# Performance work log

Measured on AMD Instinct MI355X. Metric: run time of the kernel, lower is better.

The kernel has to match this reference:

```python
import jax, jax.numpy as jnp
import numpy as np

TOP_K = 2

def setup_inputs() -> dict:
    key = jax.random.key(0)
    k0, k1, k2, k3 = jax.random.split(key, 4)
    B, S, H, I, E = 2, 2048, 1024, 1408, 8
    hidden_states = jax.random.normal(k0, (B, S, H), dtype=jnp.float32)
    router_weight = jax.random.normal(k1, (E, H), dtype=jnp.float32) * 0.02
    gate_up_proj = jax.random.normal(k2, (E, 2 * I, H), dtype=jnp.float32) * 0.02
    down_proj = jax.random.normal(k3, (E, H, I), dtype=jnp.float32) * 0.02
    return {
        "hidden_states": hidden_states,
        "router_weight": router_weight,
        "gate_up_proj": gate_up_proj,
        "down_proj": down_proj,
    }

def reference(hidden_states, router_weight, gate_up_proj, down_proj):
    B, S, H = hidden_states.shape
    E = router_weight.shape[0]
    x = hidden_states.reshape(-1, H)                       # [T, H]
    T = x.shape[0]
    # Router: logits -> float32 softmax -> top-k (matches torch: topk on probs)
    logits = x @ router_weight.T                           # [T, E]
    probs = jax.nn.softmax(logits.astype(jnp.float32), axis=-1)
    topw, topi = jax.lax.top_k(probs, TOP_K)               # [T, K]
    topw = topw.astype(x.dtype)
    # Per-token combine weights over experts (zero for non-selected experts).
    combine = jnp.zeros((T, E), dtype=x.dtype)
    combine = combine.at[jnp.arange(T)[:, None], topi].set(topw)  # [T, E]
    # Dense grouped expert compute (same math as gather-GEMM-scatter loop:
    # tokens not routed to expert e get combine weight 0).
    gu = jnp.einsum('th,eoh->teo', x, gate_up_proj)        # [T, E, 2I]
    g, u = jnp.split(gu, 2, axis=-1)                       # [T, E, I] each
    h = jax.nn.silu(g) * u                                 # [T, E, I]
    y = jnp.einsum('tei,ehi->teh', h, down_proj)           # [T, E, H]
    out = jnp.einsum('teh,te->th', y, combine)             # [T, H]
    return out.reshape(B, S, H)
```

## Files before the change

kernel.cpp:

```cpp
#include <hip/hip_runtime.h>
#include <math.h>

#define NTOK 4096
#define HDIM 1024
#define NEXP 8
#define IDIM 1408
#define TWO_I 2816
#define BM 128
#define BK 32
#define NRB 72
#define ROWCAP (NRB * BM)

typedef _Float16 f16x8 __attribute__((ext_vector_type(8)));
typedef float f32x4 __attribute__((ext_vector_type(4)));

typedef __attribute__((address_space(1))) const unsigned int gu32;
typedef __attribute__((address_space(3))) unsigned int lu32;
__device__ __forceinline__ void async16(const void* g, void* l) {
  __builtin_amdgcn_global_load_lds((gu32*)g, (lu32*)l, 16, 0, 0);
}

extern "C" __global__ void moe_init(int* counts, int* cursor, int* tok) {
  int i = blockIdx.x * 256 + threadIdx.x;
  if (i < NEXP) { counts[i] = 0; cursor[i] = 0; }
  if (i < ROWCAP) tok[i] = -1;
}

extern "C" __global__ void moe_cvt(const float* __restrict__ src, _Float16* __restrict__ dst, int n8) {
  int i = blockIdx.x * 256 + threadIdx.x;
  if (i >= n8) return;
  const float4* s = (const float4*)src + (size_t)i * 2;
  float4 a = s[0], b = s[1];
  union { _Float16 h[8]; uint4 u; } p;
  p.h[0] = (_Float16)a.x; p.h[1] = (_Float16)a.y; p.h[2] = (_Float16)a.z; p.h[3] = (_Float16)a.w;
  p.h[4] = (_Float16)b.x; p.h[5] = (_Float16)b.y; p.h[6] = (_Float16)b.z; p.h[7] = (_Float16)b.w;
  ((uint4*)dst)[i] = p.u;
}

extern "C" __global__ void moe_router(const float* __restrict__ x,
                                      const float* __restrict__ rw,
                                      int* __restrict__ topi,
                                      float* __restrict__ topw) {
  int w = threadIdx.x >> 6, lane = threadIdx.x & 63;
  int t = blockIdx.x * 4 + w;
  const float4* xp = (const float4*)(x + (size_t)t * HDIM);
  const float4* rp = (const float4*)rw;
  float acc[NEXP];
#pragma unroll
  for (int e = 0; e < NEXP; e++) acc[e] = 0.f;
#pragma unroll
  for (int i = 0; i < HDIM / 256; i++) {
    float4 xv = xp[i * 64 + lane];
#pragma unroll
    for (int e = 0; e < NEXP; e++) {
      float4 rv = rp[e * 256 + i * 64 + lane];
      acc[e] += xv.x * rv.x + xv.y * rv.y + xv.z * rv.z + xv.w * rv.w;
    }
  }
#pragma unroll
  for (int e = 0; e < NEXP; e++) {
#pragma unroll
    for (int off = 32; off > 0; off >>= 1) acc[e] += __shfl_down(acc[e], off);
  }
  if (lane == 0) {
    float m = acc[0];
    for (int e = 1; e < NEXP; e++) m = fmaxf(m, acc[e]);
    float p[NEXP], s = 0.f;
    for (int e = 0; e < NEXP; e++) { p[e] = __expf(acc[e] - m); s += p[e]; }
    float inv = 1.f / s;
    int i0 = 0; float b0 = p[0];
    for (int e = 1; e < NEXP; e++) if (p[e] > b0) { b0 = p[e]; i0 = e; }
    int i1 = -1; float b1 = -1.f;
    for (int e = 0; e < NEXP; e++) if (e != i0 && p[e] > b1) { b1 = p[e]; i1 = e; }
    topi[t * 2] = i0; topi[t * 2 + 1] = i1;
    topw[t * 2] = b0 * inv; topw[t * 2 + 1] = b1 * inv;
  }
}

extern "C" __global__ void moe_count(const int* __restrict__ topi, int* __restrict__ counts) {
  __shared__ int cnt[NEXP];
  if (threadIdx.x < NEXP) cnt[threadIdx.x] = 0;
  __syncthreads();
  int t = blockIdx.x * 256 + threadIdx.x;
  atomicAdd(&cnt[topi[t * 2]], 1);
  atomicAdd(&cnt[topi[t * 2 + 1]], 1);
  __syncthreads();
  if (threadIdx.x < NEXP) atomicAdd(&counts[threadIdx.x], cnt[threadIdx.x]);
}

extern "C" __global__ void moe_offsets(const int* __restrict__ counts, int* __restrict__ aoff) {
  if (threadIdx.x == 0) {
    int o = 0;
    aoff[0] = 0;
    for (int e = 0; e < NEXP; e++) {
      o += ((counts[e] + BM - 1) / BM) * BM;
      aoff[e + 1] = o;
    }
  }
}

extern "C" __global__ void moe_scatter(const int* __restrict__ topi, const float* __restrict__ topw,
                                       const int* __restrict__ aoff, int* __restrict__ cursor,
                                       int* __restrict__ tok, float* __restrict__ wrow,
                                       int* __restrict__ rows) {
  __shared__ int cnt[NEXP];
  __shared__ int base[NEXP];
  int tid = threadIdx.x;
  if (tid < NEXP) cnt[tid] = 0;
  __syncthreads();
  int t = blockIdx.x * 256 + tid;
  int e0 = topi[t * 2], e1 = topi[t * 2 + 1];
  int r0 = atomicAdd(&cnt[e0], 1);
  int r1 = atomicAdd(&cnt[e1], 1);
  __syncthreads();
  if (tid < NEXP) base[tid] = atomicAdd(&cursor[tid], cnt[tid]);
  __syncthreads();
  int row0 = aoff[e0] + base[e0] + r0;
  int row1 = aoff[e1] + base[e1] + r1;
  tok[row0] = t; wrow[row0] = topw[t * 2];     rows[t * 2]     = row0;
  tok[row1] = t; wrow[row1] = topw[t * 2 + 1]; rows[t * 2 + 1] = row1;
}

union SM1 {
  struct { _Float16 a[BM * BK]; _Float16 b[BM * BK]; } st;
  _Float16 ubuf[BM * 66];
};

extern "C" __global__ __launch_bounds__(256) void moe_gemm1(
    const _Float16* __restrict__ xh, const _Float16* __restrict__ guph,
    const int* __restrict__ aoff, const int* __restrict__ tok,
    _Float16* __restrict__ hbuf) {
  __shared__ __align__(16) SM1 sm;
  int row0 = blockIdx.y * BM;
  if (row0 >= aoff[8]) return;
  int e = 0;
#pragma unroll
  for (int i = 0; i < 8; i++) if (row0 >= aoff[i]) e = i;

  const int tid = threadIdx.x;
  const int lane = tid & 63, w = tid >> 6;
  const int wm = w & 1, wn = w >> 1;
  const int quad = lane >> 4, l15 = lane & 15;
  const int j = blockIdx.x;

  f32x4 acc[4][4];
#pragma unroll
  for (int im = 0; im < 4; im++)
#pragma unroll
    for (int in = 0; in < 4; in++) acc[im][in] = (f32x4){0.f, 0.f, 0.f, 0.f};

  const int lq = lane >> 2;
  const int ls = lane & 3;
  const int rA0 = w * 16 + lq, rA1 = rA0 + 64;
  int tA0 = tok[row0 + rA0]; tA0 = tA0 < 0 ? 0 : tA0;
  int tA1 = tok[row0 + rA1]; tA1 = tA1 < 0 ? 0 : tA1;
  const _Float16* gA0 = xh + (size_t)tA0 * HDIM + ls * 8;
  const _Float16* gA1 = xh + (size_t)tA1 * HDIM + ls * 8;
  const _Float16* eb = guph + (size_t)e * TWO_I * HDIM;
  const _Float16* gB0 = eb + (size_t)(j * 64 + rA0) * HDIM + ls * 8;
  const _Float16* gB1 = eb + (size_t)(IDIM + j * 64 + rA0) * HDIM + ls * 8;
  _Float16* lA0 = &sm.st.a[w * 512];
  _Float16* lA1 = &sm.st.a[(w + 4) * 512];
  _Float16* lB0 = &sm.st.b[w * 512];
  _Float16* lB1 = &sm.st.b[(w + 4) * 512];

  for (int kb = 0; kb < HDIM / BK; kb++) {
    async16(gA0, lA0); async16(gA1, lA1);
    async16(gB0, lB0); async16(gB1, lB1);
    gA0 += BK; gA1 += BK; gB0 += BK; gB1 += BK;
    __syncthreads();
    f16x8 av[4], bv[4];
#pragma unroll
    for (int im = 0; im < 4; im++)
      av[im] = *(const f16x8*)&sm.st.a[(wm * 64 + im * 16 + l15) * BK + quad * 8];
#pragma unroll
    for (int in = 0; in < 4; in++)
      bv[in] = *(const f16x8*)&sm.st.b[(wn * 64 + in * 16 + l15) * BK + quad * 8];
#pragma unroll
    for (int im = 0; im < 4; im++)
#pragma unroll
      for (int in = 0; in < 4; in++)
        acc[im][in] = __builtin_amdgcn_mfma_f32_16x16x32_f16(av[im], bv[in], acc[im][in], 0, 0, 0);
    __syncthreads();
  }

  if (wn == 1) {
#pragma unroll
    for (int im = 0; im < 4; im++)
#pragma unroll
      for (int in = 0; in < 4; in++)
#pragma unroll
        for (int r = 0; r < 4; r++)
          sm.ubuf[(wm * 64 + im * 16 + quad * 4 + r) * 66 + in * 16 + l15] = (_Float16)acc[im][in][r];
  }
  __syncthreads();
  if (wn == 0) {
#pragma unroll
    for (int im = 0; im < 4; im++)
#pragma unroll
      for (int in = 0; in < 4; in++)
#pragma unroll
        for (int r = 0; r < 4; r++) {
          float g = acc[im][in][r];
          float u = (float)sm.ubuf[(wm * 64 + im * 16 + quad * 4 + r) * 66 + in * 16 + l15];
          float hh = g / (1.f + __expf(-g)) * u;
          int row = row0 + wm * 64 + im * 16 + quad * 4 + r;
          hbuf[(size_t)row * IDIM + j * 64 + in * 16 + l15] = (_Float16)hh;
        }
  }
}

extern "C" __global__ __launch_bounds__(256) void moe_gemm2(
    const _Float16* __restrict__ hbuf, const _Float16* __restrict__ dph,
    const int* __restrict__ aoff, const float* __restrict__ wrow,
    _Float16* __restrict__ yh) {
  __shared__ __align__(16) struct { _Float16 a[BM * BK]; _Float16 b[BM * BK]; } sm;
  int row0 = blockIdx.y * BM;
  if (row0 >= aoff[8]) return;
  int e = 0;
#pragma unroll
  for (int i = 0; i < 8; i++) if (row0 >= aoff[i]) e = i;

  const int tid = threadIdx.x;
  const int lane = tid & 63, w = tid >> 6;
  const int wm = w & 1, wn = w >> 1;
  const int quad = lane >> 4, l15 = lane & 15;
  const int cb = blockIdx.x;

  f32x4 acc[4][4];
#pragma unroll
  for (int im = 0; im < 4; im++)
#pragma unroll
    for (int in = 0; in < 4; in++) acc[im][in] = (f32x4){0.f, 0.f, 0.f, 0.f};

  const int lq = lane >> 2, ls = lane & 3;
  const int rA0 = w * 16 + lq;
  const _Float16* gA0 = hbuf + (size_t)(row0 + rA0) * IDIM + ls * 8;
  const _Float16* gA1 = gA0 + (size_t)64 * IDIM;
  const _Float16* eb = dph + (size_t)e * HDIM * IDIM;
  const _Float16* gB0 = eb + (size_t)(cb * 128 + rA0) * IDIM + ls * 8;
  const _Float16* gB1 = gB0 + (size_t)64 * IDIM;
  _Float16* lA0 = &sm.a[w * 512];
  _Float16* lA1 = &sm.a[(w + 4) * 512];
  _Float16* lB0 = &sm.b[w * 512];
  _Float16* lB1 = &sm.b[(w + 4) * 512];

  for (int kb = 0; kb < IDIM / BK; kb++) {
    async16(gA0, lA0); async16(gA1, lA1);
    async16(gB0, lB0); async16(gB1, lB1);
    gA0 += BK; gA1 += BK; gB0 += BK; gB1 += BK;
    __syncthreads();
    f16x8 av[4], bv[4];
#pragma unroll
    for (int im = 0; im < 4; im++)
      av[im] = *(const f16x8*)&sm.a[(wm * 64 + im * 16 + l15) * BK + quad * 8];
#pragma unroll
    for (int in = 0; in < 4; in++)
      bv[in] = *(const f16x8*)&sm.b[(wn * 64 + in * 16 + l15) * BK + quad * 8];
#pragma unroll
    for (int im = 0; im < 4; im++)
#pragma unroll
      for (int in = 0; in < 4; in++)
        acc[im][in] = __builtin_amdgcn_mfma_f32_16x16x32_f16(av[im], bv[in], acc[im][in], 0, 0, 0);
    __syncthreads();
  }

#pragma unroll
  for (int im = 0; im < 4; im++) {
#pragma unroll
    for (int r = 0; r < 4; r++) {
      int row = row0 + wm * 64 + im * 16 + quad * 4 + r;
      float wgt = wrow[row];
#pragma unroll
      for (int in = 0; in < 4; in++) {
        int col = cb * 128 + wn * 64 + in * 16 + l15;
        yh[(size_t)row * HDIM + col] = (_Float16)(acc[im][in][r] * wgt);
      }
    }
  }
}

extern "C" __global__ void moe_combine(const _Float16* __restrict__ yh,
                                       const int* __restrict__ rows,
                                       float* __restrict__ out) {
  int i = blockIdx.x * 256 + threadIdx.x;
  int t = i >> 7, c8 = i & 127;
  int rA = rows[t * 2], rB = rows[t * 2 + 1];
  union { uint4 u; _Float16 h[8]; } pa, pb;
  pa.u = ((const uint4*)(yh + (size_t)rA * HDIM))[c8];
  pb.u = ((const uint4*)(yh + (size_t)rB * HDIM))[c8];
  float4 o0, o1;
  o0.x = (float)pa.h[0] + (float)pb.h[0]; o0.y = (float)pa.h[1] + (float)pb.h[1];
  o0.z = (float)pa.h[2] + (float)pb.h[2]; o0.w = (float)pa.h[3] + (float)pb.h[3];
  o1.x = (float)pa.h[4] + (float)pb.h[4]; o1.y = (float)pa.h[5] + (float)pb.h[5];
  o1.z = (float)pa.h[6] + (float)pb.h[6]; o1.w = (float)pa.h[7] + (float)pb.h[7];
  ((float4*)out)[(size_t)i * 2] = o0;
  ((float4*)out)[(size_t)i * 2 + 1] = o1;
}

extern "C" void kernel_launch(void* const* d_in, const int* in_sizes, int n_in,
                              void* d_out, int out_size, void* d_ws, size_t ws_size,
                              hipStream_t stream) {
  const float* x   = (const float*)d_in[0];
  const float* rw  = (const float*)d_in[1];
  const float* gup = (const float*)d_in[2];
  const float* dp  = (const float*)d_in[3];
  float* out = (float*)d_out;

  char* ws = (char*)d_ws;
  int*   counts = (int*)ws;
  int*   cursor = (int*)(ws + 64);
  int*   aoff   = (int*)(ws + 128);
  int*   topi   = (int*)(ws + 4096);
  float* topw   = (float*)(ws + 36864);
  int*   tok    = (int*)(ws + 69632);
  float* wrow   = (float*)(ws + 106496);
  int*   rows   = (int*)(ws + 143360);
  _Float16* xh   = (_Float16*)(ws + 176128);
  _Float16* guph = (_Float16*)(ws + 8564736);
  _Float16* dph  = (_Float16*)(ws + 54702080);
  _Float16* hbuf = (_Float16*)(ws + 77770752);
  _Float16* yh   = (_Float16*)(ws + 103723008);

  moe_init<<<(ROWCAP + 255) / 256, 256, 0, stream>>>(counts, cursor, tok);
  moe_router<<<NTOK / 4, 256, 0, stream>>>(x, rw, topi, topw);
  moe_count<<<NTOK / 256, 256, 0, stream>>>(topi, counts);
  moe_offsets<<<1, 64, 0, stream>>>(counts, aoff);
  moe_scatter<<<NTOK / 256, 256, 0, stream>>>(topi, topw, aoff, cursor, tok, wrow, rows);
  moe_cvt<<<(NTOK * HDIM / 8 + 255) / 256, 256, 0, stream>>>(x, xh, NTOK * HDIM / 8);
  moe_cvt<<<(NEXP * TWO_I * HDIM / 8 + 255) / 256, 256, 0, stream>>>(gup, guph, NEXP * TWO_I * HDIM / 8);
  moe_cvt<<<(NEXP * HDIM * IDIM / 8 + 255) / 256, 256, 0, stream>>>(dp, dph, NEXP * HDIM * IDIM / 8);
  moe_gemm1<<<dim3(TWO_I / 128, NRB), 256, 0, stream>>>(xh, guph, aoff, tok, hbuf);
  moe_gemm2<<<dim3(HDIM / 128, NRB), 256, 0, stream>>>(hbuf, dph, aoff, wrow, yh);
  moe_combine<<<NTOK * HDIM / 8 / 256, 256, 0, stream>>>(yh, rows, out);
}
```

Measured before the change: 336.8 us.

## Fuse activation convert into router, merge weight converts, drop offsets kernel, remap GEMM blocks

The x fp32-to-fp16 conversion now happens inside the router kernel, and the two weight conversions are merged into one launch. The offsets kernel is removed; each consumer recomputes the padded segment prefix from the counts. The GEMM grids are flattened to 1D, and block IDs are remapped so the low 3 bits pick a row-group of 9 row blocks, which is meant to spread expert work across XCDs and improve L2 reuse of expert weights. Together these cut launch overhead and one full pass over x, at the cost of some extra index arithmetic per block.

```diff
diff --git a/kernel.cpp b/kernel.cpp
--- a/kernel.cpp
+++ b/kernel.cpp
@@ -20,27 +20,39 @@
   __builtin_amdgcn_global_load_lds((gu32*)g, (lu32*)l, 16, 0, 0);
 }
 
+__device__ __forceinline__ void seg_prefix(const int* __restrict__ counts, int* aof) {
+  int o = 0; aof[0] = 0;
+#pragma unroll
+  for (int i = 0; i < 8; i++) { o += (counts[i] + 127) & ~127; aof[i + 1] = o; }
+}
+
 extern "C" __global__ void moe_init(int* counts, int* cursor, int* tok) {
   int i = blockIdx.x * 256 + threadIdx.x;
   if (i < NEXP) { counts[i] = 0; cursor[i] = 0; }
   if (i < ROWCAP) tok[i] = -1;
 }
 
-extern "C" __global__ void moe_cvt(const float* __restrict__ src, _Float16* __restrict__ dst, int n8) {
+#define NG8 (NEXP * TWO_I * HDIM / 8)
+#define ND8 (NEXP * HDIM * IDIM / 8)
+extern "C" __global__ void moe_cvtw(const float* __restrict__ gup, const float* __restrict__ dp,
+                                    _Float16* __restrict__ guph, _Float16* __restrict__ dph) {
   int i = blockIdx.x * 256 + threadIdx.x;
-  if (i >= n8) return;
-  const float4* s = (const float4*)src + (size_t)i * 2;
-  float4 a = s[0], b = s[1];
+  const float4* s; uint4* d; size_t idx;
+  if (i < NG8) { s = (const float4*)gup; d = (uint4*)guph; idx = i; }
+  else if (i < NG8 + ND8) { s = (const float4*)dp; d = (uint4*)dph; idx = i - NG8; }
+  else return;
+  float4 a = s[idx * 2], b = s[idx * 2 + 1];
   union { _Float16 h[8]; uint4 u; } p;
   p.h[0] = (_Float16)a.x; p.h[1] = (_Float16)a.y; p.h[2] = (_Float16)a.z; p.h[3] = (_Float16)a.w;
   p.h[4] = (_Float16)b.x; p.h[5] = (_Float16)b.y; p.h[6] = (_Float16)b.z; p.h[7] = (_Float16)b.w;
-  ((uint4*)dst)[i] = p.u;
+  d[idx] = p.u;
 }
 
 extern "C" __global__ void moe_router(const float* __restrict__ x,
                                       const float* __restrict__ rw,
                                       int* __restrict__ topi,
-                                      float* __restrict__ topw) {
+                                      float* __restrict__ topw,
+                                      _Float16* __restrict__ xh) {
   int w = threadIdx.x >> 6, lane = threadIdx.x & 63;
   int t = blockIdx.x * 4 + w;
   const float4* xp = (const float4*)(x + (size_t)t * HDIM);
@@ -51,6 +63,10 @@
 #pragma unroll
   for (int i = 0; i < HDIM / 256; i++) {
     float4 xv = xp[i * 64 + lane];
+    union { _Float16 h[4]; uint2 u; } pk;
+    pk.h[0] = (_Float16)xv.x; pk.h[1] = (_Float16)xv.y;
+    pk.h[2] = (_Float16)xv.z; pk.h[3] = (_Float16)xv.w;
+    *(uint2*)(xh + (size_t)t * HDIM + i * 256 + lane * 4) = pk.u;
 #pragma unroll
     for (int e = 0; e < NEXP; e++) {
       float4 rv = rp[e * 256 + i * 64 + lane];
@@ -88,23 +104,13 @@
   if (threadIdx.x < NEXP) atomicAdd(&counts[threadIdx.x], cnt[threadIdx.x]);
 }
 
-extern "C" __global__ void moe_offsets(const int* __restrict__ counts, int* __restrict__ aoff) {
-  if (threadIdx.x == 0) {
-    int o = 0;
-    aoff[0] = 0;
-    for (int e = 0; e < NEXP; e++) {
-      o += ((counts[e] + BM - 1) / BM) * BM;
-      aoff[e + 1] = o;
-    }
-  }
-}
-
 extern "C" __global__ void moe_scatter(const int* __restrict__ topi, const float* __restrict__ topw,
-                                       const int* __restrict__ aoff, int* __restrict__ cursor,
+                                       const int* __restrict__ counts, int* __restrict__ cursor,
                                        int* __restrict__ tok, float* __restrict__ wrow,
                                        int* __restrict__ rows) {
   __shared__ int cnt[NEXP];
   __shared__ int base[NEXP];
+  int aof[9]; seg_prefix(counts, aof);
   int tid = threadIdx.x;
   if (tid < NEXP) cnt[tid] = 0;
   __syncthreads();
@@ -115,8 +121,8 @@
   __syncthreads();
   if (tid < NEXP) base[tid] = atomicAdd(&cursor[tid], cnt[tid]);
   __syncthreads();
-  int row0 = aoff[e0] + base[e0] + r0;
-  int row1 = aoff[e1] + base[e1] + r1;
+  int row0 = aof[e0] + base[e0] + r0;
+  int row1 = aof[e1] + base[e1] + r1;
   tok[row0] = t; wrow[row0] = topw[t * 2];     rows[t * 2]     = row0;
   tok[row1] = t; wrow[row1] = topw[t * 2 + 1]; rows[t * 2 + 1] = row1;
 }
@@ -128,20 +134,26 @@
 
 extern "C" __global__ __launch_bounds__(256) void moe_gemm1(
     const _Float16* __restrict__ xh, const _Float16* __restrict__ guph,
-    const int* __restrict__ aoff, const int* __restrict__ tok,
+    const int* __restrict__ counts, const int* __restrict__ tok,
     _Float16* __restrict__ hbuf) {
   __shared__ __align__(16) SM1 sm;
-  int row0 = blockIdx.y * BM;
-  if (row0 >= aoff[8]) return;
+  int aof[9]; seg_prefix(counts, aof);
+  int fid = blockIdx.x;
+  int g = fid & 7, t7 = fid >> 3;
+  int jl = t7 % 11, u = t7 / 11;
+  int r = u % 9, jh = u / 9;
+  int j = jh * 11 + jl;
+  int rb = g * 9 + r;
+  int row0 = rb * BM;
+  if (row0 >= aof[8]) return;
   int e = 0;
 #pragma unroll
-  for (int i = 0; i < 8; i++) if (row0 >= aoff[i]) e = i;
+  for (int i = 0; i < 8; i++) if (row0 >= aof[i]) e = i;
 
   const int tid = threadIdx.x;
   const int lane = tid & 63, w = tid >> 6;
   const int wm = w & 1, wn = w >> 1;
   const int quad = lane >> 4, l15 = lane & 15;
-  const int j = blockIdx.x;
 
   f32x4 acc[4][4];
 #pragma unroll
@@ -190,8 +202,8 @@
 #pragma unroll
       for (int in = 0; in < 4; in++)
 #pragma unroll
-        for (int r = 0; r < 4; r++)
-          sm.ubuf[(wm * 64 + im * 16 + quad * 4 + r) * 66 + in * 16 + l15] = (_Float16)acc[im][in][r];
+        for (int r2 = 0; r2 < 4; r2++)
+          sm.ubuf[(wm * 64 + im * 16 + quad * 4 + r2) * 66 + in * 16 + l15] = (_Float16)acc[im][in][r2];
   }
   __syncthreads();
   if (wn == 0) {
@@ -200,11 +212,11 @@
 #pragma unroll
       for (int in = 0; in < 4; in++)
 #pragma unroll
-        for (int r = 0; r < 4; r++) {
-          float g = acc[im][in][r];
-          float u = (float)sm.ubuf[(wm * 64 + im * 16 + quad * 4 + r) * 66 + in * 16 + l15];
-          float hh = g / (1.f + __expf(-g)) * u;
-          int row = row0 + wm * 64 + im * 16 + quad * 4 + r;
+        for (int r2 = 0; r2 < 4; r2++) {
+          float gg = acc[im][in][r2];
+          float uu = (float)sm.ubuf[(wm * 64 + im * 16 + quad * 4 + r2) * 66 + in * 16 + l15];
+          float hh = gg / (1.f + __expf(-gg)) * uu;
+          int row = row0 + wm * 64 + im * 16 + quad * 4 + r2;
           hbuf[(size_t)row * IDIM + j * 64 + in * 16 + l15] = (_Float16)hh;
         }
   }
@@ -212,20 +224,24 @@
 
 extern "C" __global__ __launch_bounds__(256) void moe_gemm2(
     const _Float16* __restrict__ hbuf, const _Float16* __restrict__ dph,
-    const int* __restrict__ aoff, const float* __restrict__ wrow,
+    const int* __restrict__ counts, const float* __restrict__ wrow,
     _Float16* __restrict__ yh) {
   __shared__ __align__(16) struct { _Float16 a[BM * BK]; _Float16 b[BM * BK]; } sm;
-  int row0 = blockIdx.y * BM;
-  if (row0 >= aoff[8]) return;
+  int aof[9]; seg_prefix(counts, aof);
+  int fid = blockIdx.x;
+  int g = fid & 7, t7 = fid >> 3;
+  int cb = t7 & 7, r = t7 >> 3;
+  int rb = g * 9 + r;
+  int row0 = rb * BM;
+  if (row0 >= aof[8]) return;
   int e = 0;
 #pragma unroll
-  for (int i = 0; i < 8; i++) if (row0 >= aoff[i]) e = i;
+  for (int i = 0; i < 8; i++) if (row0 >= aof[i]) e = i;
 
   const int tid = threadIdx.x;
   const int lane = tid & 63, w = tid >> 6;
   const int wm = w & 1, wn = w >> 1;
   const int quad = lane >> 4, l15 = lane & 15;
-  const int cb = blockIdx.x;
 
   f32x4 acc[4][4];
 #pragma unroll
@@ -268,13 +284,13 @@
 #pragma unroll
   for (int im = 0; im < 4; im++) {
 #pragma unroll
-    for (int r = 0; r < 4; r++) {
-      int row = row0 + wm * 64 + im * 16 + quad * 4 + r;
+    for (int r2 = 0; r2 < 4; r2++) {
+      int row = row0 + wm * 64 + im * 16 + quad * 4 + r2;
       float wgt = wrow[row];
 #pragma unroll
       for (int in = 0; in < 4; in++) {
         int col = cb * 128 + wn * 64 + in * 16 + l15;
-        yh[(size_t)row * HDIM + col] = (_Float16)(acc[im][in][r] * wgt);
+        yh[(size_t)row * HDIM + col] = (_Float16)(acc[im][in][r2] * wgt);
       }
     }
   }
@@ -310,7 +326,6 @@
   char* ws = (char*)d_ws;
   int*   counts = (int*)ws;
   int*   cursor = (int*)(ws + 64);
-  int*   aoff   = (int*)(ws + 128);
   int*   topi   = (int*)(ws + 4096);
   float* topw   = (float*)(ws + 36864);
   int*   tok    = (int*)(ws + 69632);
@@ -323,14 +338,11 @@
   _Float16* yh   = (_Float16*)(ws + 103723008);
 
   moe_init<<<(ROWCAP + 255) / 256, 256, 0, stream>>>(counts, cursor, tok);
-  moe_router<<<NTOK / 4, 256, 0, stream>>>(x, rw, topi, topw);
+  moe_router<<<NTOK / 4, 256, 0, stream>>>(x, rw, topi, topw, xh);
   moe_count<<<NTOK / 256, 256, 0, stream>>>(topi, counts);
-  moe_offsets<<<1, 64, 0, stream>>>(counts, aoff);
-  moe_scatter<<<NTOK / 256, 256, 0, stream>>>(topi, topw, aoff, cursor, tok, wrow, rows);
-  moe_cvt<<<(NTOK * HDIM / 8 + 255) / 256, 256, 0, stream>>>(x, xh, NTOK * HDIM / 8);
-  moe_cvt<<<(NEXP * TWO_I * HDIM / 8 + 255) / 256, 256, 0, stream>>>(gup, guph, NEXP * TWO_I * HDIM / 8);
-  moe_cvt<<<(NEXP * HDIM * IDIM / 8 + 255) / 256, 256, 0, stream>>>(dp, dph, NEXP * HDIM * IDIM / 8);
-  moe_gemm1<<<dim3(TWO_I / 128, NRB), 256, 0, stream>>>(xh, guph, aoff, tok, hbuf);
-  moe_gemm2<<<dim3(HDIM / 128, NRB), 256, 0, stream>>>(hbuf, dph, aoff, wrow, yh);
+  moe_scatter<<<NTOK / 256, 256, 0, stream>>>(topi, topw, counts, cursor, tok, wrow, rows);
+  moe_cvtw<<<(NG8 + ND8 + 255) / 256, 256, 0, stream>>>(gup, dp, guph, dph);
+  moe_gemm1<<<8 * 22 * 9, 256, 0, stream>>>(xh, guph, counts, tok, hbuf);
+  moe_gemm2<<<8 * 8 * 9, 256, 0, stream>>>(hbuf, dph, counts, wrow, yh);
   moe_combine<<<NTOK * HDIM / 8 / 256, 256, 0, stream>>>(yh, rows, out);
 }
```

New measurement: 331.4 us. Within noise of the previous version (-1.6%).
